# Kernel tuning notes

Measured on AMD Instinct MI355X. Metric: run time of the kernel, lower is better.

The kernel has to match this reference:

```python
import jax, jax.numpy as jnp
import numpy as np

B, S, H, NH = 2, 2048, 1024, 16
DK = H // NH

def setup_inputs() -> dict:
    key = jax.random.key(0)
    ks = jax.random.split(key, 12)
    scale = 0.02
    return {
        "Q": jax.random.normal(ks[0], (B, S, H), jnp.float32),
        "K": jax.random.normal(ks[1], (B, S, H), jnp.float32),
        "V": jax.random.normal(ks[2], (B, S, H), jnp.float32),
        "attn_mask": jax.random.randint(ks[3], (B, S, S), 0, 2).astype(bool),
        "Wq": jax.random.normal(ks[4], (H, H), jnp.float32) * scale,
        "bq": jnp.zeros((H,), jnp.float32),
        "Wk": jax.random.normal(ks[5], (H, H), jnp.float32) * scale,
        "bk": jnp.zeros((H,), jnp.float32),
        "Wv": jax.random.normal(ks[6], (H, H), jnp.float32) * scale,
        "bv": jnp.zeros((H,), jnp.float32),
        "Wo": jax.random.normal(ks[7], (H, H), jnp.float32) * scale,
        "bo": jnp.zeros((H,), jnp.float32),
    }

def reference(Q, K, V, attn_mask, Wq, bq, Wk, bk, Wv, bv, Wo, bo):
    b = Q.shape[0]
    # linear projections (torch nn.Linear: x @ W.T + b), split heads -> [b, nh, s, dk]
    def proj(x, W, bias):
        return (x @ W.T + bias).reshape(b, -1, NH, DK).transpose(0, 2, 1, 3)
    q = proj(Q, Wq, bq)
    k = proj(K, Wk, bk)
    v = proj(V, Wv, bv)
    scores = jnp.einsum("bhqd,bhkd->bhqk", q, k) / jnp.sqrt(jnp.float32(DK))
    scores = jnp.where(attn_mask[:, None, :, :], jnp.float32(-1e9), scores)
    attn = jax.nn.softmax(scores, axis=-1)  # dropout prob = 0.0 (identity)
    ctx = jnp.einsum("bhqk,bhkd->bhqd", attn, v)
    ctx = ctx.transpose(0, 2, 1, 3).reshape(b, -1, NH * DK)
    return ctx @ Wo.T + bo
```

## Files before the change

kernel.cpp:

```cpp
#include <hip/hip_runtime.h>

typedef short s16x8 __attribute__((ext_vector_type(8)));
typedef float f32x4 __attribute__((ext_vector_type(4)));
typedef unsigned short u16;
typedef unsigned int u32;
typedef unsigned long long u64;

#define DEVI __device__ __forceinline__

DEVI float bf2f(u16 u){ union { u32 i; float f; } v; v.i = ((u32)u) << 16; return v.f; }
DEVI u16 f2bf(float f){ union { float f; u32 i; } v; v.f = f; u32 u = v.i;
                        return (u16)((u + 0x7fffu + ((u >> 16) & 1u)) >> 16); }

DEVI f32x4 mfma_bf16(s16x8 a, s16x8 b, f32x4 c){
  return __builtin_amdgcn_mfma_f32_16x16x32_bf16(a, b, c, 0, 0, 0);
}

#define GLDS(gp, lp) __builtin_amdgcn_global_load_lds( \
    (const __attribute__((address_space(1))) void*)(gp), \
    (__attribute__((address_space(3))) void*)(lp), 16, 0, 0)

DEVI float4 cvt8f32(const float* p){
  float4 x = *(const float4*)p;
  float4 y = *(const float4*)(p + 4);
  union { u16 t[8]; float4 f4; } u;
  u.t[0] = f2bf(x.x); u.t[1] = f2bf(x.y); u.t[2] = f2bf(x.z); u.t[3] = f2bf(x.w);
  u.t[4] = f2bf(y.x); u.t[5] = f2bf(y.y); u.t[6] = f2bf(y.z); u.t[7] = f2bf(y.w);
  return u.f4;
}

DEVI bool detect_f32(const u16* probe){
  __shared__ int dsum[4];
  const int tid = threadIdx.x;
  int bad = 0;
#pragma unroll
  for (int i = 0; i < 16; ++i){
    u16 u = probe[tid * 16 + i];
    int e = (u >> 7) & 0xFF;
    bad += (e != 0 && (e < 100 || e > 150)) ? 1 : 0;
  }
#pragma unroll
  for (int o = 1; o < 64; o <<= 1) bad += __shfl_xor(bad, o);
  if ((tid & 63) == 0) dsum[tid >> 6] = bad;
  __syncthreads();
  bool r = (dsum[0] + dsum[1] + dsum[2] + dsum[3]) > 64;
  __syncthreads();
  return r;
}

struct PrepArgs { const void* src[7]; void* dst[7]; u32 coff[8]; };

__global__ __launch_bounds__(256) void prep(PrepArgs a, const u16* probe){
  const bool f32 = detect_f32(probe);
  const u32 total = a.coff[7];
  for (u32 c = blockIdx.x * 256 + threadIdx.x; c < total; c += gridDim.x * 256){
    int s = 0;
#pragma unroll
    for (int i = 1; i < 7; ++i) s += (c >= a.coff[i]) ? 1 : 0;
    u32 lc = c - a.coff[s];
    float4 v;
    if (f32) v = cvt8f32((const float*)a.src[s] + (size_t)lc * 8);
    else     v = ((const float4*)a.src[s])[lc];
    ((float4*)a.dst[s])[lc] = v;
  }
}

__global__ __launch_bounds__(256) void maskpack(const int* __restrict__ mask,
                                                u64* __restrict__ bits){
  const int lane = threadIdx.x & 63, wid = threadIdx.x >> 6;
  const int row = blockIdx.x * 4 + wid;
  const int* mrow = mask + (size_t)row * 2048;
  for (int c = 0; c < 32; ++c){
    int v = mrow[c * 64 + lane];
    u64 w = __ballot(v != 0);
    if (lane == 0) bits[(size_t)row * 32 + c] = w;
  }
}

__global__ __launch_bounds__(256) void gemm_nt(const void* __restrict__ Av,
                                               const void* __restrict__ Bv,
                                               const void* __restrict__ biasv,
                                               void* __restrict__ outv, int mode,
                                               const u16* __restrict__ probe_in,
                                               const u16* __restrict__ oprobe){
  __shared__ u16 As[64 * 64];
  __shared__ u16 Bs[128 * 64];
  const bool in32  = detect_f32(probe_in);
  const bool aux32 = detect_f32(oprobe);
  const bool a32 = in32 && (mode != 0);
  const bool b32 = in32;
  const int tid = threadIdx.x;
  const int lane = tid & 63, wid = tid >> 6;
  const int quad = lane >> 4, l15 = lane & 15;
  const int m0 = blockIdx.y * 64, n0 = blockIdx.x * 128;
  const int wm = (wid >> 1) * 32, wn = (wid & 1) * 64;
  const int K = 1024;

  f32x4 acc[2][4];
  const f32x4 z4 = {0.f, 0.f, 0.f, 0.f};
  for (int i = 0; i < 2; ++i) for (int j = 0; j < 4; ++j) acc[i][j] = z4;

  for (int ko = 0; ko < 16; ++ko){
    const int kk = ko * 64;
    if (a32){
#pragma unroll
      for (int i = 0; i < 2; ++i){
        int g = tid * 2 + i;
        int row = g >> 3, c = g & 7;
        *(float4*)(As + row * 64 + ((c ^ (row & 7)) * 8)) =
            cvt8f32((const float*)Av + (size_t)(m0 + row) * K + kk + c * 8);
      }
    } else {
#pragma unroll
      for (int i = 0; i < 2; ++i){
        int ci = (wid * 2 + i) * 64 + lane;
        int row = ci >> 3, gcc = (ci & 7) ^ (row & 7);
        GLDS((const u16*)Av + (size_t)(m0 + row) * K + kk + gcc * 8,
             As + (size_t)(wid * 2 + i) * 512);
      }
    }
    if (b32){
#pragma unroll
      for (int i = 0; i < 4; ++i){
        int g = tid * 4 + i;
        int row = g >> 3, c = g & 7;
        *(float4*)(Bs + row * 64 + ((c ^ (row & 7)) * 8)) =
            cvt8f32((const float*)Bv + (size_t)(n0 + row) * K + kk + c * 8);
      }
    } else {
#pragma unroll
      for (int i = 0; i < 4; ++i){
        int ci = (wid * 4 + i) * 64 + lane;
        int row = ci >> 3, gcc = (ci & 7) ^ (row & 7);
        GLDS((const u16*)Bv + (size_t)(n0 + row) * K + kk + gcc * 8,
             Bs + (size_t)(wid * 4 + i) * 512);
      }
    }
    __syncthreads();
#pragma unroll
    for (int ks = 0; ks < 2; ++ks){
      s16x8 af[2], bfr[4];
#pragma unroll
      for (int mt = 0; mt < 2; ++mt){
        int row = wm + mt * 16 + l15;
        af[mt] = *(const s16x8*)(As + row * 64 + (((ks * 4 + quad) ^ (row & 7)) * 8));
      }
#pragma unroll
      for (int nt = 0; nt < 4; ++nt){
        int row = wn + nt * 16 + l15;
        bfr[nt] = *(const s16x8*)(Bs + row * 64 + (((ks * 4 + quad) ^ (row & 7)) * 8));
      }
#pragma unroll
      for (int mt = 0; mt < 2; ++mt)
#pragma unroll
        for (int nt = 0; nt < 4; ++nt)
          acc[mt][nt] = mfma_bf16(af[mt], bfr[nt], acc[mt][nt]);
    }
    __syncthreads();
  }

#pragma unroll
  for (int nt = 0; nt < 4; ++nt){
    int col = n0 + wn + nt * 16 + l15;
    float bcol = 0.f;
    if (mode != 2)
      bcol = aux32 ? ((const float*)biasv)[col] : bf2f(((const u16*)biasv)[col]);
#pragma unroll
    for (int mt = 0; mt < 2; ++mt){
#pragma unroll
      for (int r = 0; r < 4; ++r){
        int row = m0 + wm + mt * 16 + quad * 4 + r;
        float bb = bcol;
        if (mode == 2)
          bb = aux32 ? ((const float*)biasv)[row] : bf2f(((const u16*)biasv)[row]);
        float v = acc[mt][nt][r] + bb;
        size_t idx;
        if (mode == 1){
          int b = row >> 11, s = row & 2047, hh = col >> 6, d = col & 63;
          idx = (((size_t)(b * 16 + hh)) * 2048 + s) * 64 + d;
        } else if (mode == 2){
          int b = col >> 11, s = col & 2047, hh = row >> 6, d = row & 63;
          idx = (((size_t)(b * 16 + hh)) * 64 + d) * 2048 + s;
        } else {
          idx = (size_t)row * 1024 + col;
        }
        if (mode == 0 && aux32) ((float*)outv)[idx] = v;
        else                    ((u16*)outv)[idx]   = f2bf(v);
      }
    }
  }
}

__global__ __launch_bounds__(256) void attn_kernel(const u16* __restrict__ qws,
                                                   const u16* __restrict__ kws,
                                                   const u16* __restrict__ vtws,
                                                   const u32* __restrict__ mbits,
                                                   const int* __restrict__ rawmask,
                                                   int use_raw,
                                                   u16* __restrict__ ctxws){
  __shared__ u16 Ks[64 * 64];
  __shared__ u16 Vt[64 * 64];
  __shared__ u16 Ps[4][16 * 64];
  const int tid = threadIdx.x;
  const int lane = tid & 63, wid = tid >> 6;
  const int quad = lane >> 4, l15 = lane & 15;
  const int h = blockIdx.x, qt = blockIdx.y, b = blockIdx.z;
  const int q0 = qt * 64;
  const size_t bh = (size_t)(b * 16 + h) * (2048 * 64);

  s16x8 qf[2];
#pragma unroll
  for (int ks = 0; ks < 2; ++ks)
    qf[ks] = *(const s16x8*)(qws + bh + (size_t)(q0 + wid * 16 + l15) * 64 + ks * 32 + quad * 8);

  const f32x4 z4 = {0.f, 0.f, 0.f, 0.f};
  f32x4 ctx[4];
  for (int dt = 0; dt < 4; ++dt) ctx[dt] = z4;
  float lr[4] = {0.f, 0.f, 0.f, 0.f};

  for (int kt = 0; kt < 32; ++kt){
    const int k0 = kt * 64;
#pragma unroll
    for (int i = 0; i < 2; ++i){
      int ci = (wid * 2 + i) * 64 + lane;
      int row = ci >> 3, gcc = (ci & 7) ^ (row & 7);
      GLDS(kws + bh + (size_t)(k0 + row) * 64 + gcc * 8,
           Ks + (size_t)(wid * 2 + i) * 512);
      GLDS(vtws + bh + (size_t)row * 2048 + k0 + gcc * 8,
           Vt + (size_t)(wid * 2 + i) * 512);
    }
    __syncthreads();

    f32x4 s[4];
    for (int nt = 0; nt < 4; ++nt) s[nt] = z4;
#pragma unroll
    for (int ks = 0; ks < 2; ++ks){
#pragma unroll
      for (int nt = 0; nt < 4; ++nt){
        int row = nt * 16 + l15;
        s16x8 kf = *(const s16x8*)(Ks + row * 64 + (((ks * 4 + quad) ^ (row & 7)) * 8));
        s[nt] = mfma_bf16(qf[ks], kf, s[nt]);
      }
    }

#pragma unroll
    for (int r = 0; r < 4; ++r){
      int qrow = q0 + wid * 16 + quad * 4 + r;
      uint2 mw;
      if (!use_raw)
        mw = *(const uint2*)(mbits + ((size_t)(b * 2048 + qrow)) * 64 + (k0 >> 5));
      float ls = 0.f;
#pragma unroll
      for (int nt = 0; nt < 4; ++nt){
        bool masked;
        if (use_raw){
          masked = rawmask[((size_t)(b * 2048 + qrow)) * 2048 + k0 + nt * 16 + l15] != 0;
        } else {
          u32 w = (nt & 2) ? mw.y : mw.x;
          masked = (w >> ((nt & 1) * 16 + l15)) & 1u;
        }
        float sc = masked ? -1.0e9f : s[nt][r] * 0.125f;
        float pv = __expf(sc);
        s[nt][r] = pv;
        ls += pv;
      }
      lr[r] += ls;
    }

    u16* pp = &Ps[wid][0];
#pragma unroll
    for (int nt = 0; nt < 4; ++nt)
#pragma unroll
      for (int r = 0; r < 4; ++r){
        int rr = quad * 4 + r;
        int col = nt * 16 + l15;
        pp[rr * 64 + (((col >> 3) ^ (rr & 7)) * 8) + (col & 7)] = f2bf(s[nt][r]);
      }
    s16x8 pf[2];
#pragma unroll
    for (int ks = 0; ks < 2; ++ks)
      pf[ks] = *(const s16x8*)(pp + l15 * 64 + (((ks * 4 + quad) ^ (l15 & 7)) * 8));

#pragma unroll
    for (int ks = 0; ks < 2; ++ks){
#pragma unroll
      for (int dt = 0; dt < 4; ++dt){
        int d = dt * 16 + l15;
        s16x8 vf = *(const s16x8*)(Vt + d * 64 + (((ks * 4 + quad) ^ (d & 7)) * 8));
        ctx[dt] = mfma_bf16(pf[ks], vf, ctx[dt]);
      }
    }
    __syncthreads();
  }

#pragma unroll
  for (int r = 0; r < 4; ++r){
    lr[r] += __shfl_xor(lr[r], 1);
    lr[r] += __shfl_xor(lr[r], 2);
    lr[r] += __shfl_xor(lr[r], 4);
    lr[r] += __shfl_xor(lr[r], 8);
    lr[r] = 1.0f / fmaxf(lr[r], 1e-30f);
  }
#pragma unroll
  for (int dt = 0; dt < 4; ++dt){
    int d = dt * 16 + l15;
#pragma unroll
    for (int r = 0; r < 4; ++r){
      int qrow = q0 + wid * 16 + quad * 4 + r;
      ctxws[((size_t)(b * 2048 + qrow)) * 1024 + h * 64 + d] = f2bf(ctx[dt][r] * lr[r]);
    }
  }
}

extern "C" void kernel_launch(void* const* d_in, const int* in_sizes, int n_in,
                              void* d_out, int out_size, void* d_ws, size_t ws_size,
                              hipStream_t stream){
  const void* Q    = d_in[0];
  const void* Kin  = d_in[1];
  const void* Vin  = d_in[2];
  const int* mask  = (const int*)d_in[3];
  const void* Wq = d_in[4];  const void* bq = d_in[5];
  const void* Wk = d_in[6];  const void* bk = d_in[7];
  const void* Wv = d_in[8];  const void* bv = d_in[9];
  const void* Wo = d_in[10]; const void* bo = d_in[11];

  char* ws = (char*)d_ws;
  const size_t MB = 1u << 20;
  const bool small_ws = ws_size < 33 * MB;
  const bool big_ws   = ws_size >= 66 * MB;
  u32* mbits = (u32*)ws;
  const size_t base = small_ws ? 0 : MB;
  u16* qws  = (u16*)(ws + base);
  u16* kws  = (u16*)(ws + base + 8 * MB);
  u16* vtws = (u16*)(ws + base + 16 * MB);
  u16* cws  = (u16*)(ws + base + 24 * MB);
  u16* Qc  = (u16*)(ws + 33 * MB);
  u16* Kc  = (u16*)(ws + 41 * MB);
  u16* Vc  = (u16*)(ws + 49 * MB);
  u16* Wqc = (u16*)(ws + 57 * MB);
  u16* Wkc = (u16*)(ws + 59 * MB);
  u16* Wvc = (u16*)(ws + 61 * MB);
  u16* Woc = (u16*)(ws + 63 * MB);

  const u16* oprobe = (const u16*)Q;

  const void *Aq = Q, *Ak = Kin, *Av = Vin, *Gq = Wq, *Gk = Wk, *Gv = Wv, *Go = Wo;
  const u16* pin = (const u16*)Q;
  if (big_ws){
    PrepArgs pa;
    pa.src[0] = Q;  pa.src[1] = Kin; pa.src[2] = Vin;
    pa.src[3] = Wq; pa.src[4] = Wk;  pa.src[5] = Wv; pa.src[6] = Wo;
    pa.dst[0] = Qc;  pa.dst[1] = Kc;  pa.dst[2] = Vc;
    pa.dst[3] = Wqc; pa.dst[4] = Wkc; pa.dst[5] = Wvc; pa.dst[6] = Woc;
    const u32 cq = 4194304 / 8, cw = 1048576 / 8;
    pa.coff[0] = 0;
    pa.coff[1] = cq;     pa.coff[2] = 2 * cq; pa.coff[3] = 3 * cq;
    pa.coff[4] = 3 * cq + cw; pa.coff[5] = 3 * cq + 2 * cw;
    pa.coff[6] = 3 * cq + 3 * cw; pa.coff[7] = 3 * cq + 4 * cw;
    prep<<<dim3(2048), 256, 0, stream>>>(pa, (const u16*)Q);
    Aq = Qc; Ak = Kc; Av = Vc; Gq = Wqc; Gk = Wkc; Gv = Wvc; Go = Woc;
    pin = Qc;
  }

  if (!small_ws)
    maskpack<<<dim3(1024), 256, 0, stream>>>(mask, (u64*)mbits);

  gemm_nt<<<dim3(8, 64), 256, 0, stream>>>(Aq, Gq, bq, qws, 1, pin, oprobe);
  gemm_nt<<<dim3(8, 64), 256, 0, stream>>>(Ak, Gk, bk, kws, 1, pin, oprobe);
  gemm_nt<<<dim3(32, 16), 256, 0, stream>>>(Gv, Av, bv, vtws, 2, pin, oprobe);
  attn_kernel<<<dim3(16, 32, 2), 256, 0, stream>>>(qws, kws, vtws, mbits, mask,
                                                   small_ws ? 1 : 0, cws);
  gemm_nt<<<dim3(8, 64), 256, 0, stream>>>(cws, Go, bo, d_out, 0, pin, oprobe);
}
```

Baseline: 339.5 us.

## Fuse QKV projections into one batched GEMM and streamline attention softmax

```diff
diff --git a/kernel.cpp b/kernel.cpp
--- a/kernel.cpp
+++ b/kernel.cpp
@@ -8,9 +8,24 @@
 
 #define DEVI __device__ __forceinline__
 
+#if __has_builtin(__builtin_amdgcn_exp2f)
+#define EXP2F(x) __builtin_amdgcn_exp2f(x)
+#else
+#define EXP2F(x) exp2f(x)
+#endif
+
+#define QSCALE 0.1803368801111204f
+
 DEVI float bf2f(u16 u){ union { u32 i; float f; } v; v.i = ((u32)u) << 16; return v.f; }
 DEVI u16 f2bf(float f){ union { float f; u32 i; } v; v.f = f; u32 u = v.i;
                         return (u16)((u + 0x7fffu + ((u >> 16) & 1u)) >> 16); }
+DEVI u32 pack2r(float a, float b){
+  union { float f; u32 i; } ua, ub; ua.f = a; ub.f = b;
+  return ((ua.i + 0x8000u) >> 16) | ((ub.i + 0x8000u) & 0xffff0000u);
+}
+DEVI u64 pack4(float a, float b, float c, float d){
+  return (u64)f2bf(a) | ((u64)f2bf(b) << 16) | ((u64)f2bf(c) << 32) | ((u64)f2bf(d) << 48);
+}
 
 DEVI f32x4 mfma_bf16(s16x8 a, s16x8 b, f32x4 c){
   return __builtin_amdgcn_mfma_f32_16x16x32_bf16(a, b, c, 0, 0, 0);
@@ -52,16 +67,14 @@
 
 __global__ __launch_bounds__(256) void prep(PrepArgs a, const u16* probe){
   const bool f32 = detect_f32(probe);
+  if (!f32) return;
   const u32 total = a.coff[7];
   for (u32 c = blockIdx.x * 256 + threadIdx.x; c < total; c += gridDim.x * 256){
     int s = 0;
 #pragma unroll
     for (int i = 1; i < 7; ++i) s += (c >= a.coff[i]) ? 1 : 0;
     u32 lc = c - a.coff[s];
-    float4 v;
-    if (f32) v = cvt8f32((const float*)a.src[s] + (size_t)lc * 8);
-    else     v = ((const float4*)a.src[s])[lc];
-    ((float4*)a.dst[s])[lc] = v;
+    ((float4*)a.dst[s])[lc] = cvt8f32((const float*)a.src[s] + (size_t)lc * 8);
   }
 }
 
@@ -72,23 +85,125 @@
   const int* mrow = mask + (size_t)row * 2048;
   for (int c = 0; c < 32; ++c){
     int v = mrow[c * 64 + lane];
-    u64 w = __ballot(v != 0);
+    u64 w = __ballot(v == 0);
     if (lane == 0) bits[(size_t)row * 32 + c] = w;
   }
 }
 
-__global__ __launch_bounds__(256) void gemm_nt(const void* __restrict__ Av,
-                                               const void* __restrict__ Bv,
-                                               const void* __restrict__ biasv,
-                                               void* __restrict__ outv, int mode,
-                                               const u16* __restrict__ probe_in,
-                                               const u16* __restrict__ oprobe){
+struct ProjP {
+  const void* X[3];   const u16* Xc[3];
+  const void* W[3];   const u16* Wc[3];
+  const void* bias[3];
+  u16* out[3];
+  const u16* probe;
+  int conv_ok;
+};
+
+__global__ __launch_bounds__(256) void proj_gemm(ProjP p){
+  __shared__ u16 As[128 * 64];
+  __shared__ u16 Bs[128 * 64];
+  const int z = blockIdx.z;
+  const bool in32 = detect_f32(p.probe);
+  const bool f32st = in32 && !p.conv_ok;
+  const u16* Ab = (in32 && p.conv_ok) ? p.Xc[z] : (const u16*)p.X[z];
+  const u16* Wb = (in32 && p.conv_ok) ? p.Wc[z] : (const u16*)p.W[z];
+  const float* Af = (const float*)p.X[z];
+  const float* Wf = (const float*)p.W[z];
+  const int tid = threadIdx.x;
+  const int lane = tid & 63, wid = tid >> 6;
+  const int quad = lane >> 4, l15 = lane & 15;
+  const int m0 = blockIdx.y * 128, n0 = blockIdx.x * 128;
+  const int wm = (wid >> 1) * 64, wn = (wid & 1) * 64;
+  const int K = 1024;
+
+  f32x4 acc[4][4];
+  const f32x4 z4 = {0.f, 0.f, 0.f, 0.f};
+  for (int i = 0; i < 4; ++i) for (int j = 0; j < 4; ++j) acc[i][j] = z4;
+
+  for (int ko = 0; ko < 16; ++ko){
+    const int kk = ko * 64;
+    if (f32st){
+#pragma unroll
+      for (int i = 0; i < 4; ++i){
+        int g = tid * 4 + i;
+        int row = g >> 3, c = g & 7;
+        *(float4*)(As + row * 64 + ((c ^ (row & 7)) * 8)) =
+            cvt8f32(Af + (size_t)(m0 + row) * K + kk + c * 8);
+        *(float4*)(Bs + row * 64 + ((c ^ (row & 7)) * 8)) =
+            cvt8f32(Wf + (size_t)(n0 + row) * K + kk + c * 8);
+      }
+    } else {
+#pragma unroll
+      for (int i = 0; i < 4; ++i){
+        int ci = (wid * 4 + i) * 64 + lane;
+        int row = ci >> 3, gcc = (ci & 7) ^ (row & 7);
+        GLDS(Ab + (size_t)(m0 + row) * K + kk + gcc * 8, As + (size_t)(wid * 4 + i) * 512);
+        GLDS(Wb + (size_t)(n0 + row) * K + kk + gcc * 8, Bs + (size_t)(wid * 4 + i) * 512);
+      }
+    }
+    __syncthreads();
+#pragma unroll
+    for (int ks = 0; ks < 2; ++ks){
+      s16x8 af[4], bfr[4];
+#pragma unroll
+      for (int mt = 0; mt < 4; ++mt){
+        int row = wm + mt * 16 + l15;
+        af[mt] = *(const s16x8*)(As + row * 64 + (((ks * 4 + quad) ^ (row & 7)) * 8));
+      }
+#pragma unroll
+      for (int nt = 0; nt < 4; ++nt){
+        int row = wn + nt * 16 + l15;
+        bfr[nt] = *(const s16x8*)(Bs + row * 64 + (((ks * 4 + quad) ^ (row & 7)) * 8));
+      }
+#pragma unroll
+      for (int mt = 0; mt < 4; ++mt)
+#pragma unroll
+        for (int nt = 0; nt < 4; ++nt)
+          acc[mt][nt] = mfma_bf16(af[mt], bfr[nt], acc[mt][nt]);
+    }
+    __syncthreads();
+  }
+
+  u16* outp = p.out[z];
+#pragma unroll
+  for (int nt = 0; nt < 4; ++nt){
+    int col = n0 + wn + nt * 16 + l15;
+    float bv = in32 ? ((const float*)p.bias[z])[col] : bf2f(((const u16*)p.bias[z])[col]);
+#pragma unroll
+    for (int mt = 0; mt < 4; ++mt){
+      if (z == 2){
+        int srow = m0 + wm + mt * 16 + quad * 4;
+        int b = srow >> 11, s = srow & 2047, hh = col >> 6, d = col & 63;
+        size_t idx = (((size_t)(b * 16 + hh)) * 64 + d) * 2048 + s;
+        *(u64*)(outp + idx) = pack4(acc[mt][nt][0] + bv, acc[mt][nt][1] + bv,
+                                    acc[mt][nt][2] + bv, acc[mt][nt][3] + bv);
+      } else {
+#pragma unroll
+        for (int r = 0; r < 4; ++r){
+          int row = m0 + wm + mt * 16 + quad * 4 + r;
+          float v = acc[mt][nt][r] + bv;
+          if (z == 0) v *= QSCALE;
+          int b = row >> 11, s = row & 2047, hh = col >> 6, d = col & 63;
+          outp[(((size_t)(b * 16 + hh)) * 2048 + s) * 64 + d] = f2bf(v);
+        }
+      }
+    }
+  }
+}
+
+__global__ __launch_bounds__(256) void gemm_out(const u16* __restrict__ A,
+                                                const void* __restrict__ Wv,
+                                                const u16* __restrict__ Wbf,
+                                                const void* __restrict__ biasv,
+                                                void* __restrict__ outv,
+                                                const u16* __restrict__ probe,
+                                                int conv_ok){
   __shared__ u16 As[64 * 64];
   __shared__ u16 Bs[128 * 64];
-  const bool in32  = detect_f32(probe_in);
-  const bool aux32 = detect_f32(oprobe);
-  const bool a32 = in32 && (mode != 0);
-  const bool b32 = in32;
+  const bool in32 = detect_f32(probe);
+  const bool f32st = in32 && !conv_ok;
+  const u16* Wb = (in32 && conv_ok) ? Wbf : (const u16*)Wv;
+  const float* Wf = (const float*)Wv;
   const int tid = threadIdx.x;
   const int lane = tid & 63, wid = tid >> 6;
   const int quad = lane >> 4, l15 = lane & 15;
@@ -102,38 +217,26 @@
 
   for (int ko = 0; ko < 16; ++ko){
     const int kk = ko * 64;
-    if (a32){
-#pragma unroll
-      for (int i = 0; i < 2; ++i){
-        int g = tid * 2 + i;
-        int row = g >> 3, c = g & 7;
-        *(float4*)(As + row * 64 + ((c ^ (row & 7)) * 8)) =
-            cvt8f32((const float*)Av + (size_t)(m0 + row) * K + kk + c * 8);
-      }
-    } else {
-#pragma unroll
-      for (int i = 0; i < 2; ++i){
-        int ci = (wid * 2 + i) * 64 + lane;
-        int row = ci >> 3, gcc = (ci & 7) ^ (row & 7);
-        GLDS((const u16*)Av + (size_t)(m0 + row) * K + kk + gcc * 8,
-             As + (size_t)(wid * 2 + i) * 512);
-      }
-    }
-    if (b32){
+#pragma unroll
+    for (int i = 0; i < 2; ++i){
+      int ci = (wid * 2 + i) * 64 + lane;
+      int row = ci >> 3, gcc = (ci & 7) ^ (row & 7);
+      GLDS(A + (size_t)(m0 + row) * K + kk + gcc * 8, As + (size_t)(wid * 2 + i) * 512);
+    }
+    if (f32st){
 #pragma unroll
       for (int i = 0; i < 4; ++i){
         int g = tid * 4 + i;
         int row = g >> 3, c = g & 7;
         *(float4*)(Bs + row * 64 + ((c ^ (row & 7)) * 8)) =
-            cvt8f32((const float*)Bv + (size_t)(n0 + row) * K + kk + c * 8);
+            cvt8f32(Wf + (size_t)(n0 + row) * K + kk + c * 8);
       }
     } else {
 #pragma unroll
       for (int i = 0; i < 4; ++i){
         int ci = (wid * 4 + i) * 64 + lane;
         int row = ci >> 3, gcc = (ci & 7) ^ (row & 7);
-        GLDS((const u16*)Bv + (size_t)(n0 + row) * K + kk + gcc * 8,
-             Bs + (size_t)(wid * 4 + i) * 512);
+        GLDS(Wb + (size_t)(n0 + row) * K + kk + gcc * 8, Bs + (size_t)(wid * 4 + i) * 512);
       }
     }
     __syncthreads();
@@ -162,42 +265,27 @@
 #pragma unroll
   for (int nt = 0; nt < 4; ++nt){
     int col = n0 + wn + nt * 16 + l15;
-    float bcol = 0.f;
-    if (mode != 2)
-      bcol = aux32 ? ((const float*)biasv)[col] : bf2f(((const u16*)biasv)[col]);
-#pragma unroll
-    for (int mt = 0; mt < 2; ++mt){
+    float bv = in32 ? ((const float*)biasv)[col] : bf2f(((const u16*)biasv)[col]);
+#pragma unroll
+    for (int mt = 0; mt < 2; ++mt)
 #pragma unroll
       for (int r = 0; r < 4; ++r){
         int row = m0 + wm + mt * 16 + quad * 4 + r;
-        float bb = bcol;
-        if (mode == 2)
-          bb = aux32 ? ((const float*)biasv)[row] : bf2f(((const u16*)biasv)[row]);
-        float v = acc[mt][nt][r] + bb;
-        size_t idx;
-        if (mode == 1){
-          int b = row >> 11, s = row & 2047, hh = col >> 6, d = col & 63;
-          idx = (((size_t)(b * 16 + hh)) * 2048 + s) * 64 + d;
-        } else if (mode == 2){
-          int b = col >> 11, s = col & 2047, hh = row >> 6, d = row & 63;
-          idx = (((size_t)(b * 16 + hh)) * 64 + d) * 2048 + s;
-        } else {
-          idx = (size_t)row * 1024 + col;
-        }
-        if (mode == 0 && aux32) ((float*)outv)[idx] = v;
-        else                    ((u16*)outv)[idx]   = f2bf(v);
-      }
-    }
-  }
-}
-
-__global__ __launch_bounds__(256) void attn_kernel(const u16* __restrict__ qws,
-                                                   const u16* __restrict__ kws,
-                                                   const u16* __restrict__ vtws,
-                                                   const u32* __restrict__ mbits,
-                                                   const int* __restrict__ rawmask,
-                                                   int use_raw,
-                                                   u16* __restrict__ ctxws){
+        float v = acc[mt][nt][r] + bv;
+        size_t idx = (size_t)row * 1024 + col;
+        if (in32) ((float*)outv)[idx] = v;
+        else      ((u16*)outv)[idx]   = f2bf(v);
+      }
+  }
+}
+
+__global__ __launch_bounds__(256) void attn2(const u16* __restrict__ qws,
+                                             const u16* __restrict__ kws,
+                                             const u16* __restrict__ vtws,
+                                             const u64* __restrict__ mbits,
+                                             const int* __restrict__ rawmask,
+                                             int use_raw,
+                                             u16* __restrict__ ctxws){
   __shared__ u16 Ks[64 * 64];
   __shared__ u16 Vt[64 * 64];
   __shared__ u16 Ps[4][16 * 64];
@@ -207,16 +295,25 @@
   const int h = blockIdx.x, qt = blockIdx.y, b = blockIdx.z;
   const int q0 = qt * 64;
   const size_t bh = (size_t)(b * 16 + h) * (2048 * 64);
+  const int qrow = q0 + wid * 16 + l15;
 
   s16x8 qf[2];
 #pragma unroll
   for (int ks = 0; ks < 2; ++ks)
-    qf[ks] = *(const s16x8*)(qws + bh + (size_t)(q0 + wid * 16 + l15) * 64 + ks * 32 + quad * 8);
+    qf[ks] = *(const s16x8*)(qws + bh + (size_t)qrow * 64 + ks * 32 + quad * 8);
 
   const f32x4 z4 = {0.f, 0.f, 0.f, 0.f};
   f32x4 ctx[4];
   for (int dt = 0; dt < 4; ++dt) ctx[dt] = z4;
-  float lr[4] = {0.f, 0.f, 0.f, 0.f};
+  float lr = 0.f;
+
+  u16* pp = &Ps[wid][0];
+  u32 pw[4];
+#pragma unroll
+  for (int ntk = 0; ntk < 4; ++ntk)
+    pw[ntk] = l15 * 64 + (((u32)(ntk * 2 + (quad >> 1)) ^ (u32)(l15 & 7)) * 8) + (quad & 1) * 4;
+
+  const u64* mrow = mbits + ((size_t)(b * 2048 + qrow)) * 32;
 
   for (int kt = 0; kt < 32; ++kt){
     const int k0 = kt * 64;
@@ -224,91 +321,85 @@
     for (int i = 0; i < 2; ++i){
       int ci = (wid * 2 + i) * 64 + lane;
       int row = ci >> 3, gcc = (ci & 7) ^ (row & 7);
-      GLDS(kws + bh + (size_t)(k0 + row) * 64 + gcc * 8,
-           Ks + (size_t)(wid * 2 + i) * 512);
-      GLDS(vtws + bh + (size_t)row * 2048 + k0 + gcc * 8,
-           Vt + (size_t)(wid * 2 + i) * 512);
+      GLDS(kws + bh + (size_t)(k0 + row) * 64 + gcc * 8, Ks + (size_t)(wid * 2 + i) * 512);
+      GLDS(vtws + bh + (size_t)row * 2048 + k0 + gcc * 8, Vt + (size_t)(wid * 2 + i) * 512);
     }
     __syncthreads();
 
     f32x4 s[4];
-    for (int nt = 0; nt < 4; ++nt) s[nt] = z4;
-#pragma unroll
-    for (int ks = 0; ks < 2; ++ks){
-#pragma unroll
-      for (int nt = 0; nt < 4; ++nt){
-        int row = nt * 16 + l15;
+    for (int ntk = 0; ntk < 4; ++ntk) s[ntk] = z4;
+#pragma unroll
+    for (int ks = 0; ks < 2; ++ks)
+#pragma unroll
+      for (int ntk = 0; ntk < 4; ++ntk){
+        int row = ntk * 16 + l15;
         s16x8 kf = *(const s16x8*)(Ks + row * 64 + (((ks * 4 + quad) ^ (row & 7)) * 8));
-        s[nt] = mfma_bf16(qf[ks], kf, s[nt]);
-      }
-    }
-
-#pragma unroll
-    for (int r = 0; r < 4; ++r){
-      int qrow = q0 + wid * 16 + quad * 4 + r;
-      uint2 mw;
-      if (!use_raw)
-        mw = *(const uint2*)(mbits + ((size_t)(b * 2048 + qrow)) * 64 + (k0 >> 5));
-      float ls = 0.f;
-#pragma unroll
-      for (int nt = 0; nt < 4; ++nt){
-        bool masked;
-        if (use_raw){
-          masked = rawmask[((size_t)(b * 2048 + qrow)) * 2048 + k0 + nt * 16 + l15] != 0;
-        } else {
-          u32 w = (nt & 2) ? mw.y : mw.x;
-          masked = (w >> ((nt & 1) * 16 + l15)) & 1u;
+        s[ntk] = mfma_bf16(kf, qf[ks], s[ntk]);
+      }
+
+    float ls = 0.f;
+    if (!use_raw){
+      u64 w = mrow[kt] >> (quad * 4);
+      u32 wlo = (u32)w, whi = (u32)(w >> 32);
+#pragma unroll
+      for (int ntk = 0; ntk < 4; ++ntk){
+        u32 half = (ntk < 2) ? wlo : whi;
+#pragma unroll
+        for (int r = 0; r < 4; ++r){
+          float pv = EXP2F(s[ntk][r]);
+          u32 bit = (half >> ((ntk & 1) * 16 + r)) & 1u;
+          pv *= (float)bit;
+          s[ntk][r] = pv;
+          ls += pv;
         }
-        float sc = masked ? -1.0e9f : s[nt][r] * 0.125f;
-        float pv = __expf(sc);
-        s[nt][r] = pv;
-        ls += pv;
-      }
-      lr[r] += ls;
-    }
-
-    u16* pp = &Ps[wid][0];
-#pragma unroll
-    for (int nt = 0; nt < 4; ++nt)
-#pragma unroll
-      for (int r = 0; r < 4; ++r){
-        int rr = quad * 4 + r;
-        int col = nt * 16 + l15;
-        pp[rr * 64 + (((col >> 3) ^ (rr & 7)) * 8) + (col & 7)] = f2bf(s[nt][r]);
-      }
+      }
+    } else {
+#pragma unroll
+      for (int ntk = 0; ntk < 4; ++ntk)
+#pragma unroll
+        for (int r = 0; r < 4; ++r){
+          int key = k0 + ntk * 16 + quad * 4 + r;
+          int mv = rawmask[((size_t)(b * 2048 + qrow)) * 2048 + key];
+          float pv = EXP2F(s[ntk][r]);
+          pv = mv ? 0.f : pv;
+          s[ntk][r] = pv;
+          ls += pv;
+        }
+    }
+    lr += ls;
+
+#pragma unroll
+    for (int ntk = 0; ntk < 4; ++ntk){
+      uint2 t;
+      t.x = pack2r(s[ntk][0], s[ntk][1]);
+      t.y = pack2r(s[ntk][2], s[ntk][3]);
+      *(uint2*)(pp + pw[ntk]) = t;
+    }
     s16x8 pf[2];
 #pragma unroll
     for (int ks = 0; ks < 2; ++ks)
       pf[ks] = *(const s16x8*)(pp + l15 * 64 + (((ks * 4 + quad) ^ (l15 & 7)) * 8));
 
 #pragma unroll
-    for (int ks = 0; ks < 2; ++ks){
+    for (int ks = 0; ks < 2; ++ks)
 #pragma unroll
       for (int dt = 0; dt < 4; ++dt){
-        int d = dt * 16 + l15;
-        s16x8 vf = *(const s16x8*)(Vt + d * 64 + (((ks * 4 + quad) ^ (d & 7)) * 8));
-        ctx[dt] = mfma_bf16(pf[ks], vf, ctx[dt]);
-      }
-    }
-    __syncthreads();
-  }
-
-#pragma unroll
-  for (int r = 0; r < 4; ++r){
-    lr[r] += __shfl_xor(lr[r], 1);
-    lr[r] += __shfl_xor(lr[r], 2);
-    lr[r] += __shfl_xor(lr[r], 4);
-    lr[r] += __shfl_xor(lr[r], 8);
-    lr[r] = 1.0f / fmaxf(lr[r], 1e-30f);
-  }
+        int row = dt * 16 + l15;
+        s16x8 vf = *(const s16x8*)(Vt + row * 64 + (((ks * 4 + quad) ^ (row & 7)) * 8));
+        ctx[dt] = mfma_bf16(vf, pf[ks], ctx[dt]);
+      }
+    __syncthreads();
+  }
+
+  lr += __shfl_xor(lr, 16);
+  lr += __shfl_xor(lr, 32);
+  float inv = 1.0f / fmaxf(lr, 1e-30f);
+
 #pragma unroll
   for (int dt = 0; dt < 4; ++dt){
-    int d = dt * 16 + l15;
-#pragma unroll
-    for (int r = 0; r < 4; ++r){
-      int qrow = q0 + wid * 16 + quad * 4 + r;
-      ctxws[((size_t)(b * 2048 + qrow)) * 1024 + h * 64 + d] = f2bf(ctx[dt][r] * lr[r]);
-    }
+    int d0 = dt * 16 + quad * 4;
+    u64 w = pack4(ctx[dt][0] * inv, ctx[dt][1] * inv, ctx[dt][2] * inv, ctx[dt][3] * inv);
+    *(u64*)(ctxws + ((size_t)(b * 2048 + qrow)) * 1024 + h * 64 + d0) = w;
   }
 }
 
@@ -328,7 +419,7 @@
   const size_t MB = 1u << 20;
   const bool small_ws = ws_size < 33 * MB;
   const bool big_ws   = ws_size >= 66 * MB;
-  u32* mbits = (u32*)ws;
+  u64* mbits = (u64*)ws;
   const size_t base = small_ws ? 0 : MB;
   u16* qws  = (u16*)(ws + base);
   u16* kws  = (u16*)(ws + base + 8 * MB);
@@ -341,11 +432,8 @@
   u16* Wkc = (u16*)(ws + 59 * MB);
   u16* Wvc = (u16*)(ws + 61 * MB);
   u16* Woc = (u16*)(ws + 63 * MB);
-
-  const u16* oprobe = (const u16*)Q;
-
-  const void *Aq = Q, *Ak = Kin, *Av = Vin, *Gq = Wq, *Gk = Wk, *Gv = Wv, *Go = Wo;
-  const u16* pin = (const u16*)Q;
+  const u16* probe = (const u16*)Q;
+
   if (big_ws){
     PrepArgs pa;
     pa.src[0] = Q;  pa.src[1] = Kin; pa.src[2] = Vin;
@@ -354,21 +442,29 @@
     pa.dst[3] = Wqc; pa.dst[4] = Wkc; pa.dst[5] = Wvc; pa.dst[6] = Woc;
     const u32 cq = 4194304 / 8, cw = 1048576 / 8;
     pa.coff[0] = 0;
-    pa.coff[1] = cq;     pa.coff[2] = 2 * cq; pa.coff[3] = 3 * cq;
+    pa.coff[1] = cq;          pa.coff[2] = 2 * cq;      pa.coff[3] = 3 * cq;
     pa.coff[4] = 3 * cq + cw; pa.coff[5] = 3 * cq + 2 * cw;
     pa.coff[6] = 3 * cq + 3 * cw; pa.coff[7] = 3 * cq + 4 * cw;
-    prep<<<dim3(2048), 256, 0, stream>>>(pa, (const u16*)Q);
-    Aq = Qc; Ak = Kc; Av = Vc; Gq = Wqc; Gk = Wkc; Gv = Wvc; Go = Woc;
-    pin = Qc;
+    prep<<<dim3(2048), 256, 0, stream>>>(pa, probe);
   }
 
   if (!small_ws)
-    maskpack<<<dim3(1024), 256, 0, stream>>>(mask, (u64*)mbits);
-
-  gemm_nt<<<dim3(8, 64), 256, 0, stream>>>(Aq, Gq, bq, qws, 1, pin, oprobe);
-  gemm_nt<<<dim3(8, 64), 256, 0, stream>>>(Ak, Gk, bk, kws, 1, pin, oprobe);
-  gemm_nt<<<dim3(32, 16), 256, 0, stream>>>(Gv, Av, bv, vtws, 2, pin, oprobe);
-  attn_kernel<<<dim3(16, 32, 2), 256, 0, stream>>>(qws, kws, vtws, mbits, mask,
-                                                   small_ws ? 1 : 0, cws);
-  gemm_nt<<<dim3(8, 64), 256, 0, stream>>>(cws, Go, bo, d_out, 0, pin, oprobe);
-}
+    maskpack<<<dim3(1024), 256, 0, stream>>>(mask, mbits);
+
+  ProjP pp;
+  pp.X[0] = Q;  pp.X[1] = Kin; pp.X[2] = Vin;
+  pp.Xc[0] = Qc; pp.Xc[1] = Kc; pp.Xc[2] = Vc;
+  pp.W[0] = Wq; pp.W[1] = Wk; pp.W[2] = Wv;
+  pp.Wc[0] = Wqc; pp.Wc[1] = Wkc; pp.Wc[2] = Wvc;
+  pp.bias[0] = bq; pp.bias[1] = bk; pp.bias[2] = bv;
+  pp.out[0] = qws; pp.out[1] = kws; pp.out[2] = vtws;
+  pp.probe = probe;
+  pp.conv_ok = big_ws ? 1 : 0;
+  proj_gemm<<<dim3(8, 32, 3), 256, 0, stream>>>(pp);
+
+  attn2<<<dim3(16, 32, 2), 256, 0, stream>>>(qws, kws, vtws, mbits, mask,
+                                             small_ws ? 1 : 0, cws);
+
+  gemm_out<<<dim3(8, 64), 256, 0, stream>>>(cws, Wo, Woc, bo, d_out, probe,
+                                            big_ws ? 1 : 0);
+}
```

New measurement: 292.6 us. 13.8% less time.
